# Performance work log

Measured on AMD Instinct MI355X. Metric: run time of the kernel, lower is better.

## Reference

```python
import jax, jax.numpy as jnp
import numpy as np

N_CLASSES = 4
N_FEATURES = 13
N_HIDDEN = 13
N_STEPS = 100
FORGET_BIAS = 1.0


def setup_inputs() -> dict:
    key = jax.random.key(0)
    ks = jax.random.split(key, 10)
    B = 32768
    return {
        "x_input": jax.random.normal(ks[0], (B, N_STEPS, N_FEATURES), dtype=jnp.float32),
        # input projection (tf.random.normal mean=0.5 in original; values irrelevant for correctness test)
        "w_hidden": jax.random.normal(ks[1], (N_FEATURES, N_HIDDEN), dtype=jnp.float32) * 0.5 + 0.5,
        "b_hidden": jax.random.normal(ks[2], (N_HIDDEN,), dtype=jnp.float32) * 0.5 + 0.5,
        # BasicLSTMCell params: kernel [input_dim + hidden, 4*hidden], gate order (i, j, f, o)
        "lstm0_kernel": jax.random.normal(ks[3], (N_HIDDEN + N_HIDDEN, 4 * N_HIDDEN), dtype=jnp.float32) * 0.2,
        "lstm0_bias": jnp.zeros((4 * N_HIDDEN,), dtype=jnp.float32),
        "lstm1_kernel": jax.random.normal(ks[4], (N_HIDDEN + N_HIDDEN, 4 * N_HIDDEN), dtype=jnp.float32) * 0.2,
        "lstm1_bias": jnp.zeros((4 * N_HIDDEN,), dtype=jnp.float32),
        "w_output": jax.random.normal(ks[5], (N_HIDDEN, N_CLASSES), dtype=jnp.float32) * 0.5 + 0.5,
        "b_output": jax.random.normal(ks[6], (N_CLASSES,), dtype=jnp.float32) * 0.5 + 0.5,
    }


def _lstm_cell(x, c, h, kernel, bias):
    # BasicLSTMCell: z = [x; h] @ W + b, split -> i, j, f, o
    z = jnp.concatenate([x, h], axis=-1) @ kernel + bias
    i, j, f, o = jnp.split(z, 4, axis=-1)
    c_new = c * jax.nn.sigmoid(f + FORGET_BIAS) + jax.nn.sigmoid(i) * jnp.tanh(j)
    h_new = jnp.tanh(c_new) * jax.nn.sigmoid(o)
    return c_new, h_new


def reference(x_input, w_hidden, b_hidden, lstm0_kernel, lstm0_bias,
              lstm1_kernel, lstm1_bias, w_output, b_output):
    B = x_input.shape[0]
    # input projection + relu, batched over all timesteps: [B,T,F] -> [T,B,H]
    hidden = jax.nn.relu(jnp.einsum('btf,fh->bth', x_input, w_hidden) + b_hidden)
    hidden = jnp.transpose(hidden, (1, 0, 2))  # [T, B, H]

    zeros = jnp.zeros((B, N_HIDDEN), dtype=x_input.dtype)
    init = (zeros, zeros, zeros, zeros)  # (c0, h0, c1, h1)

    def step(carry, x_t):
        c0, h0, c1, h1 = carry
        c0, h0 = _lstm_cell(x_t, c0, h0, lstm0_kernel, lstm0_bias)
        c1, h1 = _lstm_cell(h0, c1, h1, lstm1_kernel, lstm1_bias)
        return (c0, h0, c1, h1), None

    (c0, h0, c1, h1), _ = jax.lax.scan(step, init, hidden)
    # last output of top LSTM layer -> output projection
    return h1 @ w_output + b_output
```

## Files before the change

kernel.cpp:

```cpp
#include <hip/hip_runtime.h>
#include <cstdint>

typedef __bf16          bf16x8 __attribute__((ext_vector_type(8)));
typedef float           f32x4  __attribute__((ext_vector_type(4)));
typedef unsigned short  u16x8  __attribute__((ext_vector_type(8)));
typedef unsigned int    u32x4  __attribute__((ext_vector_type(4)));

#define MFMA16(a,b,c) __builtin_amdgcn_mfma_f32_16x16x32_bf16((a),(b),(c),0,0,0)

__device__ __forceinline__ float rcpf(float x) { return __builtin_amdgcn_rcpf(x); }
__device__ __forceinline__ float ex2(float x)  { return __builtin_amdgcn_exp2f(x); }

__device__ __forceinline__ void split2(float v, unsigned short& hi, unsigned short& lo) {
    unsigned u = __builtin_bit_cast(unsigned, v);
    hi = (unsigned short)(u >> 16);
    float rem = v - __builtin_bit_cast(float, u & 0xffff0000u);
    lo = (unsigned short)(__builtin_bit_cast(unsigned, rem) >> 16);
}
__device__ __forceinline__ __bf16 bfbits(unsigned short b) { return __builtin_bit_cast(__bf16, b); }

__device__ __forceinline__ unsigned packhi2(float a, float b) {
    return __builtin_amdgcn_perm(__builtin_bit_cast(unsigned, b),
                                 __builtin_bit_cast(unsigned, a), 0x07060302u);
}
__device__ __forceinline__ float truncrem(float v) {
    return v - __builtin_bit_cast(float, __builtin_bit_cast(unsigned, v) & 0xffff0000u);
}


constexpr float KL = 1.4426950408889634f;

__global__ __launch_bounds__(128, 4)
void lstm_fused(const float* __restrict__ x,
                const float* __restrict__ w_hidden,
                const float* __restrict__ b_hidden,
                const float* __restrict__ k0,
                const float* __restrict__ b0,
                const float* __restrict__ k1,
                const float* __restrict__ b1,
                const float* __restrict__ w_out,
                const float* __restrict__ b_out,
                float* __restrict__ out)
{
    __shared__ __attribute__((aligned(16))) unsigned short xh_s[2][2][384];
    __shared__ __attribute__((aligned(16))) unsigned short h0_s[2][2][384];
    __shared__ __attribute__((aligned(16))) unsigned short h1_s[2][384];

    const int lane = threadIdx.x & 63;
    const int role = threadIdx.x >> 6;
    const int col  = lane & 15;
    const int q    = lane >> 4;
    const int qh   = q & 1;
    const int s0   = blockIdx.x * 16;

    {
        unsigned short* a0 = &xh_s[0][0][0];
        unsigned short* a1 = &h0_s[0][0][0];
        for (int idx = threadIdx.x; idx < 1536; idx += 128) {
            unsigned short v = ((idx % 24) == 13 && ((idx / 384) & 1) == 0)
                             ? (unsigned short)0x3F80 : (unsigned short)0;
            a0[idx] = v; a1[idx] = v;
        }
        unsigned short* a2 = &h1_s[0][0];
        for (int idx = threadIdx.x; idx < 768; idx += 128) {
            unsigned short v = ((idx % 24) == 13 && ((idx / 384) & 1) == 0)
                             ? (unsigned short)0x3F80 : (unsigned short)0;
            a2[idx] = v;
        }
    }

    const float* kp = role ? k1 : k0;
    const float* bb = role ? b1 : b0;
    bf16x8 Kh[4], Kl[4];
    #pragma unroll
    for (int g = 0; g < 4; ++g) {
        bf16x8 hv{}, lv{};
        #pragma unroll
        for (int j = 0; j < 8; ++j) {
            int k = 8 * q + j;
            float w = 0.f;
            if (col < 13) {
                if (k < 13)                 w = kp[k * 52 + 13 * g + col];
                else if (k == 13)           w = bb[13 * g + col] + (g == 2 ? 1.f : 0.f);
                else if (k >= 16 && k < 29) w = kp[(13 + k - 16) * 52 + 13 * g + col];
            }
            unsigned short h_, l_;
            split2(w, h_, l_);
            hv[j] = bfbits(h_); lv[j] = bfbits(l_);
        }
        Kh[g] = hv; Kl[g] = lv;
    }

    bf16x8 Ph{}, Pl{};
    if (role) {
        #pragma unroll
        for (int j = 0; j < 8; ++j) {
            int k = 8 * q + j;
            float w = 0.f;
            if (col < 13) {
                if (k < 13)       w = w_hidden[k * 13 + col];
                else if (k == 13) w = b_hidden[col];
            }
            unsigned short h_, l_;
            split2(w, h_, l_);
            Ph[j] = bfbits(h_); Pl[j] = bfbits(l_);
        }
    }

    const float* xrow = x + (size_t)(s0 + col) * 1300;

    auto elem = [&](float zi, float zj, float zf, float zo, float& c) -> float {
        float a   = ex2(-KL * zi);
        float b   = ex2(-2.f * KL * zj);
        float fe  = ex2(-KL * zf);
        float g   = ex2(-KL * zo);
        float opa = 1.f + a, opb = 1.f + b, opf = 1.f + fe;
        float pab = opa * opb;
        float r1  = rcpf(pab * opf);
        float cn  = fmaf(c, pab, (1.f - b) * opf) * r1;
        c = cn;
        float d   = ex2(-2.f * KL * cn);
        float r2  = rcpf((1.f + d) * (1.f + g));
        return (1.f - d) * r2;
    };

    auto cell = [&](const unsigned short* inH, const unsigned short* hidH,
                    unsigned short* outH, float* cst) {
        const unsigned short* pA = (q < 2) ? inH : hidH;
        bf16x8 ah = __builtin_bit_cast(bf16x8, *(const u16x8*)(pA + col * 24 + 8 * qh));
        bf16x8 al = __builtin_bit_cast(bf16x8, *(const u16x8*)(pA + 384 + col * 24 + 8 * qh));
        f32x4 z0 = {0.f,0.f,0.f,0.f}, z1 = z0, z2 = z0, z3 = z0;
        z0 = MFMA16(ah, Kh[0], z0); z0 = MFMA16(al, Kh[0], z0); z0 = MFMA16(ah, Kl[0], z0);
        z1 = MFMA16(ah, Kh[1], z1); z1 = MFMA16(al, Kh[1], z1); z1 = MFMA16(ah, Kl[1], z1);
        z2 = MFMA16(ah, Kh[2], z2); z2 = MFMA16(al, Kh[2], z2); z2 = MFMA16(ah, Kl[2], z2);
        z3 = MFMA16(ah, Kh[3], z3); z3 = MFMA16(al, Kh[3], z3); z3 = MFMA16(ah, Kl[3], z3);
        #pragma unroll
        for (int r = 0; r < 4; ++r) {
            float hv = elem(z0[r], z1[r], z2[r], z3[r], cst[r]);
            unsigned short hh, hl;
            split2(hv, hh, hl);
            if (col < 13) {
                outH[(4 * q + r) * 24 + col]       = hh;
                outH[384 + (4 * q + r) * 24 + col] = hl;
            }
        }
    };

    auto loadx = [&](int t, float* xv) {
        if (q < 2) {
            const float* p = xrow + t * 13 + 8 * q;
            const int lim = q ? 4 : 7;
            #pragma unroll
            for (int j = 0; j < 8; ++j) {
                int off = j > lim ? lim : j;
                xv[j] = p[off];
            }
        }
    };

    auto projc = [&](const float* xv, unsigned short* oH) {
        bf16x8 axh{}, axl{};
        if (q < 2) {
            unsigned hw0 = packhi2(xv[0], xv[1]);
            unsigned hw1 = packhi2(xv[2], xv[3]);
            unsigned hw2 = packhi2(xv[4], xv[5]);
            unsigned hw3 = packhi2(xv[6], xv[7]);
            unsigned lw0 = packhi2(truncrem(xv[0]), truncrem(xv[1]));
            unsigned lw1 = packhi2(truncrem(xv[2]), truncrem(xv[3]));
            unsigned lw2 = packhi2(truncrem(xv[4]), truncrem(xv[5]));
            unsigned lw3 = packhi2(truncrem(xv[6]), truncrem(xv[7]));
            if (q == 1) {
                hw2 = (hw2 & 0xffffu) | 0x3F800000u;
                lw2 &= 0xffffu;
                hw3 = 0u; lw3 = 0u;
            }
            u32x4 hv = {hw0, hw1, hw2, hw3};
            u32x4 lv = {lw0, lw1, lw2, lw3};
            axh = __builtin_bit_cast(bf16x8, hv);
            axl = __builtin_bit_cast(bf16x8, lv);
        }
        f32x4 zp = {0.f,0.f,0.f,0.f};
        zp = MFMA16(axh, Ph, zp);
        zp = MFMA16(axl, Ph, zp);
        zp = MFMA16(axh, Pl, zp);
        #pragma unroll
        for (int r = 0; r < 4; ++r) {
            float v = fmaxf(zp[r], 0.f);
            unsigned short hh, hl;
            split2(v, hh, hl);
            if (col < 13) {
                oH[(4 * q + r) * 24 + col]       = hh;
                oH[384 + (4 * q + r) * 24 + col] = hl;
            }
        }
    };

    float cst[4] = {0.f, 0.f, 0.f, 0.f};
    float xA[8], xB[8];

    if (role) loadx(0, xA);
    __syncthreads();
    if (role) { projc(xA, &xh_s[0][0][0]); loadx(1, xB); }
    __syncthreads();

    for (int i = 0; i < 100; i += 2) {
        if (role == 0) {
            cell(&xh_s[0][0][0], &h0_s[1][0][0], &h0_s[0][0][0], cst);
        } else {
            if (i < 98) loadx(i + 2, xA);
            if (i > 0)  cell(&h0_s[1][0][0], &h1_s[0][0], &h1_s[0][0], cst);
            projc(xB, &xh_s[1][0][0]);
        }
        __syncthreads();
        if (role == 0) {
            cell(&xh_s[1][0][0], &h0_s[0][0][0], &h0_s[1][0][0], cst);
        } else {
            if (i < 97) loadx(i + 3, xB);
            cell(&h0_s[0][0][0], &h1_s[0][0], &h1_s[0][0], cst);
            if (i < 98) projc(xA, &xh_s[0][0][0]);
        }
        __syncthreads();
    }

    if (role) {
        cell(&h0_s[1][0][0], &h1_s[0][0], &h1_s[0][0], cst);

        bf16x8 Oh{}, Ol{};
        #pragma unroll
        for (int j = 0; j < 8; ++j) {
            int k = 8 * q + j;
            float w = 0.f;
            if (col < 4) {
                if (k < 13)       w = w_out[k * 4 + col];
                else if (k == 13) w = b_out[col];
            }
            unsigned short h_, l_;
            split2(w, h_, l_);
            Oh[j] = bfbits(h_); Ol[j] = bfbits(l_);
        }
        const unsigned short* pA = &h1_s[0][0];
        bf16x8 ah = __builtin_bit_cast(bf16x8, *(const u16x8*)(pA + col * 24 + 8 * qh));
        bf16x8 al = __builtin_bit_cast(bf16x8, *(const u16x8*)(pA + 384 + col * 24 + 8 * qh));
        f32x4 zf = {0.f,0.f,0.f,0.f};
        zf = MFMA16(ah, Oh, zf);
        zf = MFMA16(al, Oh, zf);
        zf = MFMA16(ah, Ol, zf);
        if (col < 4) {
            #pragma unroll
            for (int r = 0; r < 4; ++r)
                out[(size_t)(s0 + 4 * q + r) * 4 + col] = zf[r];
        }
    }
}

extern "C" void kernel_launch(void* const* d_in, const int* in_sizes, int n_in,
                              void* d_out, int out_size, void* d_ws, size_t ws_size,
                              hipStream_t stream) {
    (void)in_sizes; (void)n_in; (void)d_ws; (void)ws_size; (void)out_size;
    lstm_fused<<<dim3(2048), dim3(128), 0, stream>>>(
        (const float*)d_in[0], (const float*)d_in[1], (const float*)d_in[2],
        (const float*)d_in[3], (const float*)d_in[4], (const float*)d_in[5],
        (const float*)d_in[6], (const float*)d_in[7], (const float*)d_in[8],
        (float*)d_out);
}
```

Baseline: 342.0 us.

## Fold sigmoid/tanh exp2 scaling into LSTM weights and split projection across roles

Prescales the LSTM kernel and bias by -log2(e), or by -2·log2(e) for the j gate, so the gate exponentials take the MFMA outputs directly. The cell state is now carried in scaled form, which saves multiplies on the recurrent critical path. The input projection is also split: the projection MFMAs still run on the layer-1 wavefront, but the ReLU and bf16 hi/lo split now happen in the layer-0 wavefront via a new shared scratch buffer. The layer-1 wavefront's cell is moved ahead of its x loads. Scaling the weights before the bf16 split changes rounding slightly, and the new buffer adds shared-memory traffic.

```diff
diff --git a/kernel.cpp b/kernel.cpp
--- a/kernel.cpp
+++ b/kernel.cpp
@@ -28,7 +28,9 @@
 }
 
 
-constexpr float KL = 1.4426950408889634f;
+constexpr float SN1 = -1.4426950408889634f;
+constexpr float SN2 = -2.8853900817779268f;
+constexpr float C2  =  2.8853900817779268f;
 
 __global__ __launch_bounds__(128, 4)
 void lstm_fused(const float* __restrict__ x,
@@ -45,6 +47,7 @@
     __shared__ __attribute__((aligned(16))) unsigned short xh_s[2][2][384];
     __shared__ __attribute__((aligned(16))) unsigned short h0_s[2][2][384];
     __shared__ __attribute__((aligned(16))) unsigned short h1_s[2][384];
+    __shared__ __attribute__((aligned(16))) float          zp_s[2][256];
 
     const int lane = threadIdx.x & 63;
     const int role = threadIdx.x >> 6;
@@ -74,6 +77,7 @@
     bf16x8 Kh[4], Kl[4];
     #pragma unroll
     for (int g = 0; g < 4; ++g) {
+        const float sg = (g == 1) ? SN2 : SN1;
         bf16x8 hv{}, lv{};
         #pragma unroll
         for (int j = 0; j < 8; ++j) {
@@ -84,6 +88,7 @@
                 else if (k == 13)           w = bb[13 * g + col] + (g == 2 ? 1.f : 0.f);
                 else if (k >= 16 && k < 29) w = kp[(13 + k - 16) * 52 + 13 * g + col];
             }
+            w *= sg;
             unsigned short h_, l_;
             split2(w, h_, l_);
             hv[j] = bfbits(h_); lv[j] = bfbits(l_);
@@ -109,17 +114,18 @@
 
     const float* xrow = x + (size_t)(s0 + col) * 1300;
 
-    auto elem = [&](float zi, float zj, float zf, float zo, float& c) -> float {
-        float a   = ex2(-KL * zi);
-        float b   = ex2(-2.f * KL * zj);
-        float fe  = ex2(-KL * zf);
-        float g   = ex2(-KL * zo);
+    auto elem = [&](float zi, float zj, float zf, float zo, float& cs) -> float {
+        float a   = ex2(zi);
+        float b   = ex2(zj);
+        float fe  = ex2(zf);
+        float g   = ex2(zo);
         float opa = 1.f + a, opb = 1.f + b, opf = 1.f + fe;
         float pab = opa * opb;
         float r1  = rcpf(pab * opf);
-        float cn  = fmaf(c, pab, (1.f - b) * opf) * r1;
-        c = cn;
-        float d   = ex2(-2.f * KL * cn);
+        float tt  = fmaf(b, C2, -C2);
+        float cn  = fmaf(cs, pab, tt * opf) * r1;
+        cs = cn;
+        float d   = ex2(cn);
         float r2  = rcpf((1.f + d) * (1.f + g));
         return (1.f - d) * r2;
     };
@@ -158,7 +164,7 @@
         }
     };
 
-    auto projc = [&](const float* xv, unsigned short* oH) {
+    auto projmfma = [&](const float* xv, float* zpo) {
         bf16x8 axh{}, axl{};
         if (q < 2) {
             unsigned hw0 = packhi2(xv[0], xv[1]);
@@ -183,6 +189,11 @@
         zp = MFMA16(axh, Ph, zp);
         zp = MFMA16(axl, Ph, zp);
         zp = MFMA16(axh, Pl, zp);
+        *(f32x4*)(zpo + lane * 4) = zp;
+    };
+
+    auto finish = [&](const float* zpi, unsigned short* oH) {
+        f32x4 zp = *(const f32x4*)(zpi + lane * 4);
         #pragma unroll
         for (int r = 0; r < 4; ++r) {
             float v = fmaxf(zp[r], 0.f);
@@ -200,24 +211,26 @@
 
     if (role) loadx(0, xA);
     __syncthreads();
-    if (role) { projc(xA, &xh_s[0][0][0]); loadx(1, xB); }
+    if (role) { projmfma(xA, &zp_s[0][0]); loadx(1, xB); }
     __syncthreads();
 
     for (int i = 0; i < 100; i += 2) {
         if (role == 0) {
+            finish(&zp_s[0][0], &xh_s[0][0][0]);
             cell(&xh_s[0][0][0], &h0_s[1][0][0], &h0_s[0][0][0], cst);
         } else {
+            if (i > 0) cell(&h0_s[1][0][0], &h1_s[0][0], &h1_s[0][0], cst);
             if (i < 98) loadx(i + 2, xA);
-            if (i > 0)  cell(&h0_s[1][0][0], &h1_s[0][0], &h1_s[0][0], cst);
-            projc(xB, &xh_s[1][0][0]);
+            projmfma(xB, &zp_s[1][0]);
         }
         __syncthreads();
         if (role == 0) {
+            finish(&zp_s[1][0], &xh_s[1][0][0]);
             cell(&xh_s[1][0][0], &h0_s[0][0][0], &h0_s[1][0][0], cst);
         } else {
+            cell(&h0_s[0][0][0], &h1_s[0][0], &h1_s[0][0], cst);
             if (i < 97) loadx(i + 3, xB);
-            cell(&h0_s[0][0][0], &h1_s[0][0], &h1_s[0][0], cst);
-            if (i < 98) projc(xA, &xh_s[0][0][0]);
+            if (i < 98) projmfma(xA, &zp_s[0][0]);
         }
         __syncthreads();
     }
```

Measured after the change: 355.7 us. 1.04x slower.
